# Kernel optimization log

Measured on AMD Instinct MI355X. Metric: run time of the kernel, lower is better.

The kernel has to match this reference:

```python
import jax, jax.numpy as jnp
import numpy as np

B, S, DIM, HID, E, TOPK = 32, 512, 1024, 4096, 8, 2
CF = 1.0


def setup_inputs() -> dict:
    key = jax.random.key(0)
    ks = jax.random.split(key, 12)
    sc = 0.02
    return {
        "router_input": jax.random.normal(ks[0], (B, S, DIM), jnp.float32),
        "x": jax.random.normal(ks[1], (B, S, DIM), jnp.float32),
        "noise": jax.random.normal(ks[2], (B, E), jnp.float32),
        # router params (stored [in,out])
        "Wg": jax.random.normal(ks[3], (DIM, E), jnp.float32) * sc,
        "bg": jnp.zeros((E,), jnp.float32),
        "Wn": jax.random.normal(ks[4], (DIM, E), jnp.float32) * sc,
        "bn": jnp.zeros((E,), jnp.float32),
        # expert MLP params, stacked over experts
        "W1": jax.random.normal(ks[5], (E, DIM, HID), jnp.float32) * sc,
        "b1": jnp.zeros((E, HID), jnp.float32),
        "W2": jax.random.normal(ks[6], (E, HID, DIM), jnp.float32) * sc,
        "b2": jnp.zeros((E, DIM), jnp.float32),
    }


def reference(router_input, x, noise, Wg, bg, Wn, bn, W1, b1, W2, b2):
    b, s, d = x.shape
    e = Wg.shape[1]
    # ---- noisy top-k router (per-sample: mean over sequence) ----
    ri = router_input.mean(axis=1)                      # [B, D]
    logits = ri @ Wg + bg                               # [B, E]
    noise_logits = ri @ Wn + bn                         # [B, E]
    noisy = logits + noise * jax.nn.softplus(noise_logits)
    top_vals, top_idx = jax.lax.top_k(noisy, TOPK)      # [B, K]
    # softmax over -inf-masked logits == softmax over the kept top-k values
    gate = jax.nn.softmax(top_vals, axis=-1)            # [B, K]

    flat_e = top_idx.reshape(-1)                        # [N] expert id per (sample,k) pair
    flat_w = gate.reshape(-1)                           # [N]
    sample_ids = jnp.repeat(jnp.arange(b), TOPK)        # [N]
    n = b * TOPK
    capacity = max(int(n / e * CF), 1)

    # ---- capacity drop: keep first `capacity` pairs per expert in sorted order ----
    order = jnp.argsort(flat_e, stable=True)            # stable sort by expert id
    sorted_e = flat_e[order]
    rank_in_expert = jnp.arange(n) - jnp.searchsorted(sorted_e, sorted_e, side="left")
    keep = jnp.zeros((n,), bool).at[order].set(rank_in_expert < capacity)

    # ---- per-pair expert MLP via gathered expert weights (grouped GEMM) ----
    xp = x[sample_ids]                                  # [N, S, D]
    h = jnp.einsum("psd,pdh->psh", xp, W1[flat_e]) + b1[flat_e][:, None, :]
    h = jax.nn.gelu(h, approximate=False)               # exact GELU (torch nn.GELU)
    y = jnp.einsum("psh,phd->psd", h, W2[flat_e]) + b2[flat_e][:, None, :]

    # ---- weight by gate, zero dropped pairs, combine back per sample ----
    y = y * (flat_w * keep.astype(y.dtype))[:, None, None]
    return jax.ops.segment_sum(y, sample_ids, num_segments=b)  # [B, S, D]
```

## Files before the change

kernel.cpp:

```cpp
#include <hip/hip_runtime.h>
#include <hip/hip_bf16.h>
#include <math.h>

#define B_    32
#define S_    512
#define DIM_  1024
#define HID_  4096
#define E_    8
#define TOPK_ 2
#define CAP_  8
#define NSLOT_ 64

typedef __bf16 bf16_t;
typedef bf16_t bf16x8 __attribute__((ext_vector_type(8)));
typedef float  f32x4  __attribute__((ext_vector_type(4)));

__device__ __forceinline__ ushort f2bf(float f) {
    union { float f; unsigned u; } v; v.f = f;
    unsigned r = (v.u + 0x7fffu + ((v.u >> 16) & 1u)) >> 16;
    return (ushort)r;
}

__device__ __forceinline__ void async_cp16(const ushort* g, ushort* l) {
    __builtin_amdgcn_global_load_lds(
        (const __attribute__((address_space(1))) unsigned int*)g,
        (__attribute__((address_space(3))) unsigned int*)l, 16, 0, 0);
}

__global__ void k_mean(const float* __restrict__ rin, float* __restrict__ ri) {
    int b = blockIdx.x;
    int d4 = threadIdx.x;
    const float4* p = (const float4*)(rin + (size_t)b * S_ * DIM_) + d4;
    float4 acc = {0.f, 0.f, 0.f, 0.f};
    for (int s = 0; s < S_; ++s) {
        float4 v = p[(size_t)s * (DIM_ / 4)];
        acc.x += v.x; acc.y += v.y; acc.z += v.z; acc.w += v.w;
    }
    const float inv = 1.0f / (float)S_;
    float4 o = {acc.x * inv, acc.y * inv, acc.z * inv, acc.w * inv};
    ((float4*)(ri + (size_t)b * DIM_))[d4] = o;
}

__global__ void k_router(const float* __restrict__ ri, const float* __restrict__ noise,
                         const float* __restrict__ Wg, const float* __restrict__ bg,
                         const float* __restrict__ Wn, const float* __restrict__ bn,
                         int* __restrict__ slot_sample, float* __restrict__ slot_gate) {
    __shared__ float noisy[B_][E_];
    __shared__ int   top_i[B_][TOPK_];
    __shared__ float top_g[B_][TOPK_];
    int t = threadIdx.x;
    int b = t >> 3, e = t & 7;
    {
        float accg = 0.f, accn = 0.f;
        const float* r = ri + (size_t)b * DIM_;
        for (int d = 0; d < DIM_; ++d) {
            float rv = r[d];
            accg += rv * Wg[d * E_ + e];
            accn += rv * Wn[d * E_ + e];
        }
        accg += bg[e]; accn += bn[e];
        float sp = (accn > 20.f) ? accn : log1pf(expf(accn));
        noisy[b][e] = accg + noise[b * E_ + e] * sp;
    }
    __syncthreads();
    if (t < B_) {
        float v1 = -INFINITY, v2 = -INFINITY; int i1 = 0, i2 = 0;
        for (int ee = 0; ee < E_; ++ee) {
            float v = noisy[t][ee];
            if (v > v1)      { v2 = v1; i2 = i1; v1 = v; i1 = ee; }
            else if (v > v2) { v2 = v; i2 = ee; }
        }
        float g2 = expf(v2 - v1);
        float s = 1.f + g2;
        top_i[t][0] = i1; top_i[t][1] = i2;
        top_g[t][0] = 1.f / s; top_g[t][1] = g2 / s;
    }
    if (t < NSLOT_) { slot_sample[t] = -1; slot_gate[t] = 0.f; }
    __syncthreads();
    if (t == 0) {
        int cnt[E_];
        for (int ee = 0; ee < E_; ++ee) cnt[ee] = 0;
        for (int p = 0; p < B_ * TOPK_; ++p) {
            int bb = p >> 1, kk = p & 1;
            int ee = top_i[bb][kk];
            int c = cnt[ee]++;
            if (c < CAP_) {
                slot_sample[ee * CAP_ + c] = bb;
                slot_gate[ee * CAP_ + c]   = top_g[bb][kk];
            }
        }
    }
}

__global__ void k_cvt_x(const float* __restrict__ x, ushort* __restrict__ xb, int n8) {
    int i = blockIdx.x * blockDim.x + threadIdx.x;
    if (i >= n8) return;
    const float4* p = (const float4*)x + (size_t)i * 2;
    float4 a = p[0], b = p[1];
    union { ushort s[8]; uint4 v; } u;
    u.s[0] = f2bf(a.x); u.s[1] = f2bf(a.y); u.s[2] = f2bf(a.z); u.s[3] = f2bf(a.w);
    u.s[4] = f2bf(b.x); u.s[5] = f2bf(b.y); u.s[6] = f2bf(b.z); u.s[7] = f2bf(b.w);
    ((uint4*)xb)[i] = u.v;
}

__global__ void k_transpose_cvt(const float* __restrict__ W, ushort* __restrict__ Wt,
                                int K, int N) {
    __shared__ float tile[64][65];
    size_t eoff = (size_t)blockIdx.z * K * N;
    const float* Win = W + eoff;
    ushort* Wout = Wt + eoff;
    int n0 = blockIdx.x * 64, k0 = blockIdx.y * 64;
    int t = threadIdx.x;
    int r = t >> 4;
    int c4 = (t & 15) << 2;
#pragma unroll
    for (int i = 0; i < 4; ++i) {
        float4 v = *(const float4*)(Win + (size_t)(k0 + r + i * 16) * N + n0 + c4);
        tile[r + i * 16][c4 + 0] = v.x;
        tile[r + i * 16][c4 + 1] = v.y;
        tile[r + i * 16][c4 + 2] = v.z;
        tile[r + i * 16][c4 + 3] = v.w;
    }
    __syncthreads();
#pragma unroll
    for (int i = 0; i < 4; ++i) {
        int nn = r + i * 16;
        ushort4 o;
        o.x = f2bf(tile[c4 + 0][nn]);
        o.y = f2bf(tile[c4 + 1][nn]);
        o.z = f2bf(tile[c4 + 2][nn]);
        o.w = f2bf(tile[c4 + 3][nn]);
        *(ushort4*)(Wout + (size_t)(n0 + nn) * K + k0 + c4) = o;
    }
}

__device__ __forceinline__ void gemm_mainloop(
    const ushort* __restrict__ Abase, int lda,
    const ushort* __restrict__ Bbase, int ldb,
    int K, ushort* lds_a, ushort* lds_b, f32x4 acc[4][4]) {
    int tid = threadIdx.x;
    int wave = tid >> 6, lane = tid & 63;
    int wm = wave & 1, wn = wave >> 1;
    int quad = lane >> 4, mr = lane & 15;
    int r_lo = lane >> 2;
    int kp   = (lane & 3) << 3;
    const ushort* a_g0 = Abase + (size_t)(wave * 16 + r_lo) * lda + kp;
    const ushort* a_g1 = Abase + (size_t)((wave + 4) * 16 + r_lo) * lda + kp;
    const ushort* b_g0 = Bbase + (size_t)(wave * 16 + r_lo) * ldb + kp;
    const ushort* b_g1 = Bbase + (size_t)((wave + 4) * 16 + r_lo) * ldb + kp;
    ushort* a_l0 = lds_a + wave * 512;
    ushort* a_l1 = lds_a + (wave + 4) * 512;
    ushort* b_l0 = lds_b + wave * 512;
    ushort* b_l1 = lds_b + (wave + 4) * 512;
    for (int k0 = 0; k0 < K; k0 += 32) {
        __syncthreads();
        async_cp16(a_g0 + k0, a_l0);
        async_cp16(a_g1 + k0, a_l1);
        async_cp16(b_g0 + k0, b_l0);
        async_cp16(b_g1 + k0, b_l1);
        __syncthreads();
        bf16x8 af[4], bfr[4];
#pragma unroll
        for (int i = 0; i < 4; ++i)
            af[i] = *(const bf16x8*)&lds_a[(wm * 64 + i * 16 + mr) * 32 + quad * 8];
#pragma unroll
        for (int i = 0; i < 4; ++i)
            bfr[i] = *(const bf16x8*)&lds_b[(wn * 64 + i * 16 + mr) * 32 + quad * 8];
#pragma unroll
        for (int i = 0; i < 4; ++i)
#pragma unroll
            for (int j = 0; j < 4; ++j)
                acc[i][j] = __builtin_amdgcn_mfma_f32_16x16x32_bf16(af[i], bfr[j], acc[i][j], 0, 0, 0);
    }
}

__global__ __launch_bounds__(256, 2) void k_gemm1(
    const ushort* __restrict__ xb, const ushort* __restrict__ w1t,
    const float* __restrict__ b1, const int* __restrict__ slot_sample,
    ushort* __restrict__ H) {
    __shared__ ushort As[128 * 32];
    __shared__ ushort Bs[128 * 32];
    int slot = blockIdx.z;
    int samp = slot_sample[slot];
    if (samp < 0) return;
    int e = slot >> 3;
    int mt = blockIdx.y, nt = blockIdx.x;
    const ushort* Abase = xb + ((size_t)samp * S_ + mt * 128) * DIM_;
    const ushort* Bbase = w1t + (size_t)e * HID_ * DIM_ + (size_t)(nt * 128) * DIM_;
    f32x4 acc[4][4];
#pragma unroll
    for (int i = 0; i < 4; ++i)
#pragma unroll
        for (int j = 0; j < 4; ++j) acc[i][j] = (f32x4){0.f, 0.f, 0.f, 0.f};
    gemm_mainloop(Abase, DIM_, Bbase, DIM_, DIM_, As, Bs, acc);
    int wave = threadIdx.x >> 6, lane = threadIdx.x & 63;
    int wm = wave & 1, wn = wave >> 1, quad = lane >> 4, mr = lane & 15;
    ushort* Hrow = H + ((size_t)slot * S_ + mt * 128) * HID_ + nt * 128;
#pragma unroll
    for (int j = 0; j < 4; ++j) {
        int nl = wn * 64 + j * 16 + mr;
        float bias = b1[e * HID_ + nt * 128 + nl];
#pragma unroll
        for (int i = 0; i < 4; ++i) {
#pragma unroll
            for (int r = 0; r < 4; ++r) {
                int ml = wm * 64 + i * 16 + quad * 4 + r;
                float v = acc[i][j][r] + bias;
                float g = 0.5f * v * (1.0f + erff(v * 0.70710678118654752f));
                Hrow[(size_t)ml * HID_ + nl] = f2bf(g);
            }
        }
    }
}

__global__ __launch_bounds__(256, 2) void k_gemm2(
    const ushort* __restrict__ H, const ushort* __restrict__ w2t,
    const float* __restrict__ b2, const int* __restrict__ slot_sample,
    const float* __restrict__ slot_gate, float* __restrict__ out) {
    __shared__ ushort As[128 * 32];
    __shared__ ushort Bs[128 * 32];
    int slot = blockIdx.z;
    int samp = slot_sample[slot];
    if (samp < 0) return;
    int e = slot >> 3;
    float gate = slot_gate[slot];
    int mt = blockIdx.y, nt = blockIdx.x;
    const ushort* Abase = H + ((size_t)slot * S_ + mt * 128) * HID_;
    const ushort* Bbase = w2t + (size_t)e * DIM_ * HID_ + (size_t)(nt * 128) * HID_;
    f32x4 acc[4][4];
#pragma unroll
    for (int i = 0; i < 4; ++i)
#pragma unroll
        for (int j = 0; j < 4; ++j) acc[i][j] = (f32x4){0.f, 0.f, 0.f, 0.f};
    gemm_mainloop(Abase, HID_, Bbase, HID_, HID_, As, Bs, acc);
    int wave = threadIdx.x >> 6, lane = threadIdx.x & 63;
    int wm = wave & 1, wn = wave >> 1, quad = lane >> 4, mr = lane & 15;
    float* Orow = out + ((size_t)samp * S_ + mt * 128) * DIM_ + nt * 128;
#pragma unroll
    for (int j = 0; j < 4; ++j) {
        int nl = wn * 64 + j * 16 + mr;
        float bias = b2[e * DIM_ + nt * 128 + nl];
#pragma unroll
        for (int i = 0; i < 4; ++i) {
#pragma unroll
            for (int r = 0; r < 4; ++r) {
                int ml = wm * 64 + i * 16 + quad * 4 + r;
                float v = acc[i][j][r] + bias;
                atomicAdd(&Orow[(size_t)ml * DIM_ + nl], v * gate);
            }
        }
    }
}

extern "C" void kernel_launch(void* const* d_in, const int* in_sizes, int n_in,
                              void* d_out, int out_size, void* d_ws, size_t ws_size,
                              hipStream_t stream) {
    const float* rin   = (const float*)d_in[0];
    const float* x     = (const float*)d_in[1];
    const float* noise = (const float*)d_in[2];
    const float* Wg    = (const float*)d_in[3];
    const float* bg    = (const float*)d_in[4];
    const float* Wn    = (const float*)d_in[5];
    const float* bn    = (const float*)d_in[6];
    const float* W1    = (const float*)d_in[7];
    const float* b1    = (const float*)d_in[8];
    const float* W2    = (const float*)d_in[9];
    const float* b2    = (const float*)d_in[10];
    float* out = (float*)d_out;

    char* ws = (char*)d_ws;
    float*  ri          = (float*)ws;
    int*    slot_sample = (int*)(ws + 131072);
    float*  slot_gate   = (float*)(ws + 131072 + 256);
    ushort* xb  = (ushort*)(ws + 135168);
    ushort* w1t = (ushort*)(ws + 135168 + 33554432);
    ushort* w2t = (ushort*)(ws + 135168 + 33554432 + 67108864);
    ushort* H   = (ushort*)(ws + 135168 + 33554432 + 2 * 67108864);

    hipMemsetAsync(d_out, 0, (size_t)out_size * sizeof(float), stream);
    k_mean<<<B_, 256, 0, stream>>>(rin, ri);
    k_router<<<1, 256, 0, stream>>>(ri, noise, Wg, bg, Wn, bn, slot_sample, slot_gate);
    k_cvt_x<<<(B_ * S_ * DIM_ / 8 + 255) / 256, 256, 0, stream>>>(x, xb, B_ * S_ * DIM_ / 8);
    k_transpose_cvt<<<dim3(HID_ / 64, DIM_ / 64, E_), 256, 0, stream>>>(W1, w1t, DIM_, HID_);
    k_transpose_cvt<<<dim3(DIM_ / 64, HID_ / 64, E_), 256, 0, stream>>>(W2, w2t, HID_, DIM_);
    k_gemm1<<<dim3(HID_ / 128, S_ / 128, NSLOT_), 256, 0, stream>>>(xb, w1t, b1, slot_sample, H);
    k_gemm2<<<dim3(DIM_ / 128, S_ / 128, NSLOT_), 256, 0, stream>>>(H, w2t, b2, slot_sample, slot_gate, out);
}
```

Baseline: 1.194 ms.

## Parallelize router mean/logits and make gemm2 sample-major without atomics

Splits the sequence-mean into a partial-sum kernel plus a final reduction across many blocks, and computes router logits with one block per sample and a shared-memory reduction instead of a single block. gemm2 is reorganised so each block owns one output sample and accumulates both of its expert slots in registers, rescaling by the gate ratio between passes. It then stores results directly, which removes the output memset and the float atomics. This adds extra launches and a gate-ratio division that could lose precision for tiny gates. Scratch buffers reuse the H region before gemm1 overwrites it.

```diff
diff --git a/kernel.cpp b/kernel.cpp
--- a/kernel.cpp
+++ b/kernel.cpp
@@ -27,13 +27,23 @@
         (__attribute__((address_space(3))) unsigned int*)l, 16, 0, 0);
 }
 
-__global__ void k_mean(const float* __restrict__ rin, float* __restrict__ ri) {
-    int b = blockIdx.x;
+__global__ void k_mean_p(const float* __restrict__ rin, float* __restrict__ part) {
+    int p = blockIdx.x, b = blockIdx.y;
     int d4 = threadIdx.x;
-    const float4* p = (const float4*)(rin + (size_t)b * S_ * DIM_) + d4;
+    const float4* base = (const float4*)(rin + ((size_t)b * S_ + p * 32) * DIM_) + d4;
     float4 acc = {0.f, 0.f, 0.f, 0.f};
-    for (int s = 0; s < S_; ++s) {
-        float4 v = p[(size_t)s * (DIM_ / 4)];
+    for (int s = 0; s < 32; ++s) {
+        float4 v = base[(size_t)s * (DIM_ / 4)];
+        acc.x += v.x; acc.y += v.y; acc.z += v.z; acc.w += v.w;
+    }
+    ((float4*)(part + (size_t)(b * 16 + p) * DIM_))[d4] = acc;
+}
+
+__global__ void k_mean_f(const float* __restrict__ part, float* __restrict__ ri) {
+    int b = blockIdx.x, d4 = threadIdx.x;
+    float4 acc = {0.f, 0.f, 0.f, 0.f};
+    for (int p = 0; p < 16; ++p) {
+        float4 v = ((const float4*)(part + (size_t)(b * 16 + p) * DIM_))[d4];
         acc.x += v.x; acc.y += v.y; acc.z += v.z; acc.w += v.w;
     }
     const float inv = 1.0f / (float)S_;
@@ -41,32 +51,46 @@
     ((float4*)(ri + (size_t)b * DIM_))[d4] = o;
 }
 
-__global__ void k_router(const float* __restrict__ ri, const float* __restrict__ noise,
-                         const float* __restrict__ Wg, const float* __restrict__ bg,
-                         const float* __restrict__ Wn, const float* __restrict__ bn,
-                         int* __restrict__ slot_sample, float* __restrict__ slot_gate) {
-    __shared__ float noisy[B_][E_];
+__global__ void k_router_logits(const float* __restrict__ ri, const float* __restrict__ noise,
+                                const float* __restrict__ Wg, const float* __restrict__ bg,
+                                const float* __restrict__ Wn, const float* __restrict__ bn,
+                                float* __restrict__ noisy) {
+    __shared__ float rrow[DIM_];
+    __shared__ float pg[256], pn[256];
+    int b = blockIdx.x, t = threadIdx.x;
+    ((float4*)rrow)[t] = ((const float4*)(ri + (size_t)b * DIM_))[t];
+    __syncthreads();
+    int e = t & 7, c = t >> 3;
+    float ag = 0.f, an = 0.f;
+    for (int i = 0; i < 32; ++i) {
+        float rv = rrow[c * 32 + i];
+        ag += rv * Wg[(c * 32 + i) * E_ + e];
+        an += rv * Wn[(c * 32 + i) * E_ + e];
+    }
+    pg[t] = ag; pn[t] = an;
+    __syncthreads();
+    for (int off = 128; off >= 8; off >>= 1) {
+        if (t < off) { pg[t] += pg[t + off]; pn[t] += pn[t + off]; }
+        __syncthreads();
+    }
+    if (t < E_) {
+        float lg = pg[t] + bg[t];
+        float ln = pn[t] + bn[t];
+        float sp = (ln > 20.f) ? ln : log1pf(expf(ln));
+        noisy[b * E_ + t] = lg + noise[b * E_ + t] * sp;
+    }
+}
+
+__global__ void k_router_assign(const float* __restrict__ noisy,
+                                int* __restrict__ slot_sample, float* __restrict__ slot_gate,
+                                int* __restrict__ sample_slot, float* __restrict__ sample_gate) {
     __shared__ int   top_i[B_][TOPK_];
     __shared__ float top_g[B_][TOPK_];
     int t = threadIdx.x;
-    int b = t >> 3, e = t & 7;
-    {
-        float accg = 0.f, accn = 0.f;
-        const float* r = ri + (size_t)b * DIM_;
-        for (int d = 0; d < DIM_; ++d) {
-            float rv = r[d];
-            accg += rv * Wg[d * E_ + e];
-            accn += rv * Wn[d * E_ + e];
-        }
-        accg += bg[e]; accn += bn[e];
-        float sp = (accn > 20.f) ? accn : log1pf(expf(accn));
-        noisy[b][e] = accg + noise[b * E_ + e] * sp;
-    }
-    __syncthreads();
     if (t < B_) {
         float v1 = -INFINITY, v2 = -INFINITY; int i1 = 0, i2 = 0;
         for (int ee = 0; ee < E_; ++ee) {
-            float v = noisy[t][ee];
+            float v = noisy[t * E_ + ee];
             if (v > v1)      { v2 = v1; i2 = i1; v1 = v; i1 = ee; }
             else if (v > v2) { v2 = v; i2 = ee; }
         }
@@ -75,7 +99,8 @@
         top_i[t][0] = i1; top_i[t][1] = i2;
         top_g[t][0] = 1.f / s; top_g[t][1] = g2 / s;
     }
-    if (t < NSLOT_) { slot_sample[t] = -1; slot_gate[t] = 0.f; }
+    if (t < NSLOT_)      { slot_sample[t] = -1; slot_gate[t] = 0.f; }
+    if (t < B_ * TOPK_)  { sample_slot[t] = -1; sample_gate[t] = 0.f; }
     __syncthreads();
     if (t == 0) {
         int cnt[E_];
@@ -85,8 +110,11 @@
             int ee = top_i[bb][kk];
             int c = cnt[ee]++;
             if (c < CAP_) {
-                slot_sample[ee * CAP_ + c] = bb;
-                slot_gate[ee * CAP_ + c]   = top_g[bb][kk];
+                int slot = ee * CAP_ + c;
+                slot_sample[slot] = bb;
+                slot_gate[slot]   = top_g[bb][kk];
+                sample_slot[bb * TOPK_ + kk] = slot;
+                sample_gate[bb * TOPK_ + kk] = top_g[bb][kk];
             }
         }
     }
@@ -215,38 +243,53 @@
 
 __global__ __launch_bounds__(256, 2) void k_gemm2(
     const ushort* __restrict__ H, const ushort* __restrict__ w2t,
-    const float* __restrict__ b2, const int* __restrict__ slot_sample,
-    const float* __restrict__ slot_gate, float* __restrict__ out) {
+    const float* __restrict__ b2, const int* __restrict__ sample_slot,
+    const float* __restrict__ sample_gate, float* __restrict__ out) {
     __shared__ ushort As[128 * 32];
     __shared__ ushort Bs[128 * 32];
-    int slot = blockIdx.z;
-    int samp = slot_sample[slot];
-    if (samp < 0) return;
-    int e = slot >> 3;
-    float gate = slot_gate[slot];
+    int b = blockIdx.z;
+    int sl0 = sample_slot[b * TOPK_ + 0], sl1 = sample_slot[b * TOPK_ + 1];
+    float ga0 = sample_gate[b * TOPK_ + 0], ga1 = sample_gate[b * TOPK_ + 1];
+    if (sl0 < 0) { sl0 = sl1; ga0 = ga1; sl1 = -1; }
     int mt = blockIdx.y, nt = blockIdx.x;
-    const ushort* Abase = H + ((size_t)slot * S_ + mt * 128) * HID_;
-    const ushort* Bbase = w2t + (size_t)e * DIM_ * HID_ + (size_t)(nt * 128) * HID_;
     f32x4 acc[4][4];
 #pragma unroll
     for (int i = 0; i < 4; ++i)
 #pragma unroll
         for (int j = 0; j < 4; ++j) acc[i][j] = (f32x4){0.f, 0.f, 0.f, 0.f};
-    gemm_mainloop(Abase, HID_, Bbase, HID_, HID_, As, Bs, acc);
+    if (sl0 >= 0) {
+        int e0 = sl0 >> 3;
+        gemm_mainloop(H + ((size_t)sl0 * S_ + mt * 128) * HID_, HID_,
+                      w2t + (size_t)e0 * DIM_ * HID_ + (size_t)(nt * 128) * HID_, HID_,
+                      HID_, As, Bs, acc);
+    }
+    if (sl1 >= 0) {
+        float ratio = ga0 / ga1;
+#pragma unroll
+        for (int i = 0; i < 4; ++i)
+#pragma unroll
+            for (int j = 0; j < 4; ++j) acc[i][j] = acc[i][j] * ratio;
+        int e1 = sl1 >> 3;
+        gemm_mainloop(H + ((size_t)sl1 * S_ + mt * 128) * HID_, HID_,
+                      w2t + (size_t)e1 * DIM_ * HID_ + (size_t)(nt * 128) * HID_, HID_,
+                      HID_, As, Bs, acc);
+    }
+    float gfin = (sl1 >= 0) ? ga1 : ((sl0 >= 0) ? ga0 : 0.f);
     int wave = threadIdx.x >> 6, lane = threadIdx.x & 63;
     int wm = wave & 1, wn = wave >> 1, quad = lane >> 4, mr = lane & 15;
-    float* Orow = out + ((size_t)samp * S_ + mt * 128) * DIM_ + nt * 128;
+    float* Orow = out + ((size_t)b * S_ + mt * 128) * DIM_ + nt * 128;
 #pragma unroll
     for (int j = 0; j < 4; ++j) {
         int nl = wn * 64 + j * 16 + mr;
-        float bias = b2[e * DIM_ + nt * 128 + nl];
+        float bias = 0.f;
+        if (sl0 >= 0) bias += ga0 * b2[(sl0 >> 3) * DIM_ + nt * 128 + nl];
+        if (sl1 >= 0) bias += ga1 * b2[(sl1 >> 3) * DIM_ + nt * 128 + nl];
 #pragma unroll
         for (int i = 0; i < 4; ++i) {
 #pragma unroll
             for (int r = 0; r < 4; ++r) {
                 int ml = wm * 64 + i * 16 + quad * 4 + r;
-                float v = acc[i][j][r] + bias;
-                atomicAdd(&Orow[(size_t)ml * DIM_ + nl], v * gate);
+                Orow[(size_t)ml * DIM_ + nl] = acc[i][j][r] * gfin + bias;
             }
         }
     }
@@ -271,18 +314,25 @@
     char* ws = (char*)d_ws;
     float*  ri          = (float*)ws;
     int*    slot_sample = (int*)(ws + 131072);
-    float*  slot_gate   = (float*)(ws + 131072 + 256);
+    float*  slot_gate   = (float*)(ws + 131328);
+    int*    sample_slot = (int*)(ws + 131584);
+    float*  sample_gate = (float*)(ws + 131840);
     ushort* xb  = (ushort*)(ws + 135168);
     ushort* w1t = (ushort*)(ws + 135168 + 33554432);
     ushort* w2t = (ushort*)(ws + 135168 + 33554432 + 67108864);
     ushort* H   = (ushort*)(ws + 135168 + 33554432 + 2 * 67108864);
-
-    hipMemsetAsync(d_out, 0, (size_t)out_size * sizeof(float), stream);
-    k_mean<<<B_, 256, 0, stream>>>(rin, ri);
-    k_router<<<1, 256, 0, stream>>>(ri, noise, Wg, bg, Wn, bn, slot_sample, slot_gate);
+    float* part  = (float*)H;
+    float* noisy = (float*)((char*)H + 2097152);
+
+    k_mean_p<<<dim3(16, B_), 256, 0, stream>>>(rin, part);
+    k_mean_f<<<B_, 256, 0, stream>>>(part, ri);
+    k_router_logits<<<B_, 256, 0, stream>>>(ri, noise, Wg, bg, Wn, bn, noisy);
+    k_router_assign<<<1, 256, 0, stream>>>(noisy, slot_sample, slot_gate,
+                                           sample_slot, sample_gate);
     k_cvt_x<<<(B_ * S_ * DIM_ / 8 + 255) / 256, 256, 0, stream>>>(x, xb, B_ * S_ * DIM_ / 8);
     k_transpose_cvt<<<dim3(HID_ / 64, DIM_ / 64, E_), 256, 0, stream>>>(W1, w1t, DIM_, HID_);
     k_transpose_cvt<<<dim3(DIM_ / 64, HID_ / 64, E_), 256, 0, stream>>>(W2, w2t, HID_, DIM_);
     k_gemm1<<<dim3(HID_ / 128, S_ / 128, NSLOT_), 256, 0, stream>>>(xb, w1t, b1, slot_sample, H);
-    k_gemm2<<<dim3(DIM_ / 128, S_ / 128, NSLOT_), 256, 0, stream>>>(H, w2t, b2, slot_sample, slot_gate, out);
-}
+    k_gemm2<<<dim3(DIM_ / 128, S_ / 128, B_), 256, 0, stream>>>(H, w2t, b2, sample_slot,
+                                                                sample_gate, out);
+}
```

Measured after the change: 1.137 ms. 1.05x faster.
